# Kernel optimization log

Measured on AMD Instinct MI355X. Metric: run time of the kernel, lower is better.

Reference implementation:

```python
import jax, jax.numpy as jnp
import numpy as np

HQ, HKV, HD = 32, 8, 64
G = HQ // HKV
SCALE = HD ** -0.5


def _rope(x, offset=0):
    # x: [B, L, H, hd], interleaved-pair rotary as in the torch module
    B, L, H, hd = x.shape
    inv = 1.0 / (10000.0 ** (jnp.arange(0, hd, 2, dtype=jnp.float32) / hd))  # [hd/2]
    pos = jnp.arange(offset, offset + L, dtype=jnp.float32)
    f = pos[:, None] * inv[None, :]                     # [L, hd/2]
    c = jnp.cos(f)[None, :, None, :]
    s = jnp.sin(f)[None, :, None, :]
    x1, x2 = x[..., 0::2], x[..., 1::2]
    out = jnp.stack([x1 * c - x2 * s, x1 * s + x2 * c], axis=-1)  # [B,L,H,hd/2,2]
    return out.reshape(x.shape)


def setup_inputs() -> dict:
    key = jax.random.key(0)
    ks = jax.random.split(key, 5)
    B, L, D = 2, 2048, 2048
    w = 0.02
    return {
        "x": jax.random.normal(ks[0], (B, L, D), dtype=jnp.float32),
        "Wq": jax.random.normal(ks[1], (HQ * HD, D), dtype=jnp.float32) * w,
        "Wk": jax.random.normal(ks[2], (HKV * HD, D), dtype=jnp.float32) * w,
        "Wv": jax.random.normal(ks[3], (HKV * HD, D), dtype=jnp.float32) * w,
        "Wo": jax.random.normal(ks[4], (D, HQ * HD), dtype=jnp.float32) * w,
    }


def reference(x, Wq, Wk, Wv, Wo):
    B, L, D = x.shape
    q = (x @ Wq.T).reshape(B, L, HQ, HD)
    k = (x @ Wk.T).reshape(B, L, HKV, HD)
    v = (x @ Wv.T).reshape(B, L, HKV, HD)
    q = _rope(q)
    k = _rope(k)
    # GQA via broadcasting instead of repeat_interleave:
    # q head i attends kv head i // G -> group axis g
    qh = q.transpose(0, 2, 1, 3).reshape(B, HKV, G, L, HD)  # [B,Hkv,G,L,hd]
    kh = k.transpose(0, 2, 1, 3)                             # [B,Hkv,L,hd]
    vh = v.transpose(0, 2, 1, 3)
    attn = jnp.einsum("bkgqd,bkld->bkgql", qh, kh) * SCALE
    causal = jnp.arange(L)[:, None] >= jnp.arange(L)[None, :]  # kv_len == L
    attn = jnp.where(causal[None, None, None], attn, -jnp.inf)
    p = jax.nn.softmax(attn, axis=-1)
    out = jnp.einsum("bkgql,bkld->bkgqd", p, vh)             # [B,Hkv,G,L,hd]
    out = out.reshape(B, HQ, L, HD).transpose(0, 2, 1, 3).reshape(B, L, HQ * HD)
    return out @ Wo.T
```

## Files before the change

kernel.cpp:

```cpp
#include <hip/hip_runtime.h>
#include <hip/hip_bf16.h>
#include <hip/hip_fp16.h>

typedef unsigned short u16;
typedef __attribute__((ext_vector_type(8))) short     bf16x8;
typedef __attribute__((ext_vector_type(4))) float     f32x4;
typedef __attribute__((ext_vector_type(4))) _Float16  f16x4;
typedef __attribute__((ext_vector_type(8))) _Float16  f16x8;
typedef __attribute__((ext_vector_type(4))) u16       u16x4;

static constexpr int B_ = 2, L_ = 2048, D_ = 2048;
static constexpr int HQ_ = 32, HD_ = 64;
static constexpr int M_ = B_ * L_;
static constexpr int KVD_ = 512;
static constexpr int NQKV_ = D_ + 2 * KVD_;
static constexpr float QSCALE_ = 0.125f * 1.44269504f;

__device__ __forceinline__ u16 f2bf(float x) {
  union { float f; unsigned u; } c; c.f = x;
  unsigned r = c.u + 0x7FFFu + ((c.u >> 16) & 1u);
  return (u16)(r >> 16);
}
__device__ __forceinline__ float bf2f(u16 x) {
  union { unsigned u; float f; } c; c.u = ((unsigned)x) << 16;
  return c.f;
}

__global__ void cvt5_kernel(const float* __restrict__ s0, const float* __restrict__ s1,
                            const float* __restrict__ s2, const float* __restrict__ s3,
                            const float* __restrict__ s4, u16* __restrict__ dst,
                            long p0, long p1, long p2, long p3, long ntot4) {
  long i = (long)blockIdx.x * blockDim.x + threadIdx.x;
  if (i >= ntot4) return;
  const float* src; long lo;
  if (i < p0)      { src = s0; lo = i; }
  else if (i < p1) { src = s1; lo = i - p0; }
  else if (i < p2) { src = s2; lo = i - p1; }
  else if (i < p3) { src = s3; lo = i - p2; }
  else             { src = s4; lo = i - p3; }
  float4 v = ((const float4*)src)[lo];
  u16x4 w;
  w[0] = f2bf(v.x); w[1] = f2bf(v.y); w[2] = f2bf(v.z); w[3] = f2bf(v.w);
  ((u16x4*)dst)[i] = w;
}

__device__ __forceinline__ void gld_lds16(const void* g, void* l) {
  __builtin_amdgcn_global_load_lds((const __attribute__((address_space(1))) void*)g,
                                   (__attribute__((address_space(3))) void*)l, 16, 0, 0);
}

template <int OUTM>
__global__ __launch_bounds__(256) void gemm_bt(const u16* __restrict__ A,
                                               const u16* __restrict__ Bm,
                                               void* __restrict__ C,
                                               int M, int N, int K) {
  __shared__ u16 As[128 * 32];
  __shared__ u16 Bs[128 * 32];
  const int tid  = threadIdx.x;
  const int lane = tid & 63;
  const int wave = tid >> 6;
  const int wr = wave >> 1, wc = wave & 1;
  const long bm = (long)blockIdx.y * 128;
  const long bn = (long)blockIdx.x * 128;

  f32x4 acc[4][4] = {};

  const u16* ag = A + (bm + wave * 32 + (lane >> 2)) * (long)K + (lane & 3) * 8;
  const u16* bg = Bm + (bn + wave * 32 + (lane >> 2)) * (long)K + (lane & 3) * 8;
  u16* asl0 = &As[wave * 1024];
  u16* asl1 = &As[wave * 1024 + 512];
  u16* bsl0 = &Bs[wave * 1024];
  u16* bsl1 = &Bs[wave * 1024 + 512];

  for (int k0 = 0; k0 < K; k0 += 32) {
    __syncthreads();
    gld_lds16(ag + k0, asl0);
    gld_lds16(ag + k0 + 16 * (long)K, asl1);
    gld_lds16(bg + k0, bsl0);
    gld_lds16(bg + k0 + 16 * (long)K, bsl1);
    __syncthreads();
    bf16x8 af[4], bf[4];
    const int kx = (lane >> 4) * 8;
#pragma unroll
    for (int m = 0; m < 4; ++m)
      af[m] = *(const bf16x8*)&As[(wr * 64 + m * 16 + (lane & 15)) * 32 + kx];
#pragma unroll
    for (int n = 0; n < 4; ++n)
      bf[n] = *(const bf16x8*)&Bs[(wc * 64 + n * 16 + (lane & 15)) * 32 + kx];
#pragma unroll
    for (int m = 0; m < 4; ++m)
#pragma unroll
      for (int n = 0; n < 4; ++n)
        acc[m][n] = __builtin_amdgcn_mfma_f32_16x16x32_bf16(af[m], bf[n], acc[m][n], 0, 0, 0);
  }

  const int cw = lane & 15;
  const int rg = (lane >> 4) * 4;
#pragma unroll
  for (int m = 0; m < 4; ++m) {
    const long row0 = bm + wr * 64 + m * 16 + rg;
#pragma unroll
    for (int n = 0; n < 4; ++n) {
      const long col = bn + wc * 64 + n * 16 + cw;
      if (OUTM == 2) {
#pragma unroll
        for (int j = 0; j < 4; ++j)
          ((float*)C)[(row0 + j) * (long)N + col] = acc[m][n][j];
      } else {
        u16* qb = (u16*)C;
        u16* kb = qb + (long)M_ * D_;
        _Float16* vt = (_Float16*)(kb + (long)M_ * KVD_);
        if (bn < D_) {
#pragma unroll
          for (int j = 0; j < 4; ++j)
            qb[(row0 + j) * (long)D_ + col] = f2bf(acc[m][n][j]);
        } else if (bn < D_ + KVD_) {
#pragma unroll
          for (int j = 0; j < 4; ++j)
            kb[(row0 + j) * (long)KVD_ + (col - D_)] = f2bf(acc[m][n][j]);
        } else {
          f16x4 w;
#pragma unroll
          for (int j = 0; j < 4; ++j) w[j] = (_Float16)acc[m][n][j];
          const long off3 = (row0 >> 11) * ((long)KVD_ * L_) + (col - D_ - KVD_) * (long)L_ + (row0 & (L_ - 1));
          *(f16x4*)(vt + off3) = w;
        }
      }
    }
  }
}

__global__ void rope_kernel(u16* __restrict__ buf, int npairs_row, float outscale, int total) {
  int idx = blockIdx.x * blockDim.x + threadIdx.x;
  if (idx >= total) return;
  int row = idx / npairs_row;
  int cp  = idx - row * npairs_row;
  int i   = cp & 31;
  int pos = row & (L_ - 1);
  float f = (float)pos * __expf(-(float)(2 * i) * (9.210340372f / 64.f));
  float s, c;
  __sincosf(f, &s, &c);
  long off = (long)row * (npairs_row * 2) + (cp >> 5) * 64 + (i << 1);
  float x1 = bf2f(buf[off]), x2 = bf2f(buf[off + 1]);
  buf[off]     = f2bf((x1 * c - x2 * s) * outscale);
  buf[off + 1] = f2bf((x1 * s + x2 * c) * outscale);
}

__device__ __forceinline__ void sm_step(f32x4 (&s)[4], f16x4 (&pb)[4], float& l_run,
                                        int kv0, int qbase, int qq, int kg) {
  if (kv0 + 63 > qbase) {
    const int qrow = qbase + qq;
    const int kb0 = kv0 + 4 * kg;
#pragma unroll
    for (int ks = 0; ks < 4; ++ks)
#pragma unroll
      for (int j = 0; j < 4; ++j)
        s[ks][j] = (kb0 + ks * 16 + j <= qrow) ? s[ks][j] : -INFINITY;
  }
  float ps[4];
#pragma unroll
  for (int ks = 0; ks < 4; ++ks) {
    const float p0 = exp2f(s[ks][0]), p1 = exp2f(s[ks][1]);
    const float p2 = exp2f(s[ks][2]), p3 = exp2f(s[ks][3]);
    pb[ks][0] = (_Float16)p0; pb[ks][1] = (_Float16)p1;
    pb[ks][2] = (_Float16)p2; pb[ks][3] = (_Float16)p3;
    ps[ks] = (p0 + p1) + (p2 + p3);
  }
  l_run += (ps[0] + ps[1]) + (ps[2] + ps[3]);
}

__device__ __forceinline__ void pv_step(const f16x4 (&va)[4][4], const f16x4 (&pb)[4],
                                        f32x4 (&acc)[4]) {
  __builtin_amdgcn_s_setprio(1);
#pragma unroll
  for (int ks = 0; ks < 4; ++ks)
#pragma unroll
    for (int dt = 0; dt < 4; ++dt)
      acc[dt] = __builtin_amdgcn_mfma_f32_16x16x16f16(va[ks][dt], pb[ks], acc[dt], 0, 0, 0);
  __builtin_amdgcn_s_setprio(0);
}

__global__ __launch_bounds__(256) void attn_kernel(const u16* __restrict__ Q,
                                                   const u16* __restrict__ Kb,
                                                   const _Float16* __restrict__ VT,
                                                   u16* __restrict__ O) {
  const int bid = blockIdx.x;
  const int kvh = bid & 7;
  const int idx = bid >> 3;
  const int q4  = idx & 15;
  const int hh  = (idx >> 4) & 3;
  const int b   = idx >> 6;
  const int s4  = idx >> 5;
  int qblk;
  if (s4 == 0)      qblk = q4;
  else if (s4 == 1) qblk = 15 - q4;
  else if (s4 == 2) qblk = (q4 + 8) & 15;
  else              qblk = (7 - q4) & 15;
  const int h = kvh * 4 + hh;

  const int tid = threadIdx.x, lane = tid & 63, wave = tid >> 6;
  const int qq = lane & 15, kg = lane >> 4;

  __shared__ u16      Ks[2][2][64 * 64];
  __shared__ _Float16 Vs[2][2][64 * 64];

  const int q0 = qblk * 128 + wave * 32;
  bf16x8 qf[2][2];
#pragma unroll
  for (int f = 0; f < 2; ++f) {
    const u16* qp = Q + (long)(b * L_ + q0 + f * 16 + qq) * D_ + h * 64 + kg * 8;
    qf[f][0] = *(const bf16x8*)qp;
    qf[f][1] = *(const bf16x8*)(qp + 32);
  }
  f32x4 acc0[4] = {}, acc1[4] = {};
  float l0 = 0.f, l1 = 0.f;
  const int ntiles = qblk + 1;

  const u16*      kbase = Kb + (long)b * L_ * KVD_ + kvh * 64;
  const _Float16* vbase = VT + (long)b * ((long)KVD_ * L_) + (long)(kvh * 64) * L_;

  auto stage = [&](int buf, int t) {
    const long kv0 = (long)t * 128;
#pragma unroll
    for (int v = 0; v < 2; ++v) {
#pragma unroll
      for (int i = 0; i < 2; ++i) {
        const int c   = tid + i * 256;
        const int row = c >> 3;
        const int s16 = (c & 7) ^ (row & 7);
        gld_lds16(kbase + (kv0 + v * 64 + row) * KVD_ + s16 * 8, (u16*)&Ks[buf][v][0] + c * 8);
        gld_lds16(vbase + (long)row * L_ + kv0 + v * 64 + s16 * 8, (_Float16*)&Vs[buf][v][0] + c * 8);
      }
    }
  };

  stage(0, 0);
  __syncthreads();

  for (int t = 0; t < ntiles; ++t) {
    const int buf = t & 1;
    if (t + 1 < ntiles) stage(buf ^ 1, t + 1);

    const int sw = (qq & 7) << 4;
#pragma unroll
    for (int v = 0; v < 2; ++v) {
      const int kv0 = t * 128 + v * 64;
      const char* ksb = (const char*)&Ks[buf][v][0];
      const char* vsb = (const char*)&Vs[buf][v][0];

      bf16x8 kf[4][2];
#pragma unroll
      for (int ks = 0; ks < 4; ++ks) {
        const int rowb = (ks * 16 + qq) * 128;
        kf[ks][0] = *(const bf16x8*)(ksb + rowb + ((kg * 16) ^ sw));
        kf[ks][1] = *(const bf16x8*)(ksb + rowb + ((kg * 16 + 64) ^ sw));
      }
      f16x4 va[4][4];
#pragma unroll
      for (int ks = 0; ks < 4; ++ks)
#pragma unroll
        for (int dt = 0; dt < 4; ++dt)
          va[ks][dt] = *(const f16x4*)(vsb + (dt * 16 + qq) * 128 + ((ks * 32 + kg * 8) ^ sw));

      f32x4 s[4];
      f16x4 pb[4];
#pragma unroll
      for (int ks = 0; ks < 4; ++ks) {
        f32x4 z = {};
        z = __builtin_amdgcn_mfma_f32_16x16x32_bf16(kf[ks][0], qf[0][0], z, 0, 0, 0);
        z = __builtin_amdgcn_mfma_f32_16x16x32_bf16(kf[ks][1], qf[0][1], z, 0, 0, 0);
        s[ks] = z;
      }
      sm_step(s, pb, l0, kv0, q0, qq, kg);
      pv_step(va, pb, acc0);
#pragma unroll
      for (int ks = 0; ks < 4; ++ks) {
        f32x4 z = {};
        z = __builtin_amdgcn_mfma_f32_16x16x32_bf16(kf[ks][0], qf[1][0], z, 0, 0, 0);
        z = __builtin_amdgcn_mfma_f32_16x16x32_bf16(kf[ks][1], qf[1][1], z, 0, 0, 0);
        s[ks] = z;
      }
      sm_step(s, pb, l1, kv0, q0 + 16, qq, kg);
      pv_step(va, pb, acc1);
    }

    __syncthreads();
  }

#pragma unroll
  for (int f = 0; f < 2; ++f) {
    const f32x4* accw = f ? acc1 : acc0;
    float lr = f ? l1 : l0;
    lr += __shfl_xor(lr, 16);
    lr += __shfl_xor(lr, 32);
    const float inv_l = 1.f / lr;
    const long row = (long)(b * L_ + q0 + f * 16 + qq);
#pragma unroll
    for (int dt = 0; dt < 4; ++dt) {
      u16x4 w2;
#pragma unroll
      for (int j = 0; j < 4; ++j) w2[j] = f2bf(accw[dt][j] * inv_l);
      *(u16x4*)(O + row * D_ + h * 64 + dt * 16 + 4 * kg) = w2;
    }
  }
}

extern "C" void kernel_launch(void* const* d_in, const int* in_sizes, int n_in,
                              void* d_out, int out_size, void* d_ws, size_t ws_size,
                              hipStream_t stream) {
  const float* x  = (const float*)d_in[0];
  const float* Wq = (const float*)d_in[1];
  const float* Wk = (const float*)d_in[2];
  const float* Wv = (const float*)d_in[3];
  const float* Wo = (const float*)d_in[4];
  float* out = (float*)d_out;
  char* ws = (char*)d_ws;
  size_t off = 0;
  auto alloc = [&](size_t bytes) -> void* {
    void* p = ws + off; off += (bytes + 255) & ~(size_t)255; return p;
  };
  u16* x_bf  = (u16*)alloc((size_t)M_ * D_ * 2);
  u16* wq_bf = (u16*)alloc((size_t)D_ * D_ * 2);
  u16* wk_bf = (u16*)alloc((size_t)KVD_ * D_ * 2);
  u16* wv_bf = (u16*)alloc((size_t)KVD_ * D_ * 2);
  u16* wo_bf = (u16*)alloc((size_t)D_ * D_ * 2);
  u16* qb = (u16*)alloc((size_t)M_ * D_ * 2);
  u16* kb = (u16*)alloc((size_t)M_ * KVD_ * 2);
  _Float16* vt = (_Float16*)alloc((size_t)M_ * KVD_ * 2);
  u16* ao = (u16*)alloc((size_t)M_ * D_ * 2);

  {
    const long q0 = (long)M_ * D_ / 4;
    const long q1 = q0 + (long)D_ * D_ / 4;
    const long q2 = q1 + (long)KVD_ * D_ / 4;
    const long q3 = q2 + (long)KVD_ * D_ / 4;
    const long qt = q3 + (long)D_ * D_ / 4;
    cvt5_kernel<<<(int)((qt + 255) / 256), 256, 0, stream>>>(x, Wq, Wk, Wv, Wo, x_bf,
                                                             q0, q1, q2, q3, qt);
  }

  dim3 blk(256);
  gemm_bt<4><<<dim3(NQKV_ / 128, M_ / 128), blk, 0, stream>>>(x_bf, wq_bf, qb, M_, NQKV_, D_);

  {
    int totq = M_ * (D_ / 2);
    rope_kernel<<<(totq + 255) / 256, blk, 0, stream>>>(qb, D_ / 2, QSCALE_, totq);
    int totk = M_ * (KVD_ / 2);
    rope_kernel<<<(totk + 255) / 256, blk, 0, stream>>>(kb, KVD_ / 2, 1.0f, totk);
  }

  attn_kernel<<<dim3(1024), dim3(256), 0, stream>>>(qb, kb, vt, ao);

  gemm_bt<2><<<dim3(D_ / 128, M_ / 128), blk, 0, stream>>>(ao, wo_bf, (void*)out, M_, D_, D_);
}
```

Before: 256.3 us.

## Fuse RoPE into QKV GEMM epilogue and double attention query block size

Applies the rotary embedding and query scaling inside the QKV GEMM epilogue, pairing adjacent columns with a lane shuffle, and removes the two standalone rope kernels. This avoids an extra read-modify-write pass over Q and K and two launches. The attention kernel now uses 512-thread blocks covering 256 query rows, so each K/V tile staged into shared memory serves twice as many queries. Waves whose causal range ends early skip compute but still join the barriers. Load balance changes to a simple per-batch reversed ordering over 512 blocks, which may hurt tail balance.

```diff
diff --git a/kernel.cpp b/kernel.cpp
--- a/kernel.cpp
+++ b/kernel.cpp
@@ -20,10 +20,6 @@
   union { float f; unsigned u; } c; c.f = x;
   unsigned r = c.u + 0x7FFFu + ((c.u >> 16) & 1u);
   return (u16)(r >> 16);
-}
-__device__ __forceinline__ float bf2f(u16 x) {
-  union { unsigned u; float f; } c; c.u = ((unsigned)x) << 16;
-  return c.f;
 }
 
 __global__ void cvt5_kernel(const float* __restrict__ s0, const float* __restrict__ s1,
@@ -110,14 +106,21 @@
         u16* qb = (u16*)C;
         u16* kb = qb + (long)M_ * D_;
         _Float16* vt = (_Float16*)(kb + (long)M_ * KVD_);
-        if (bn < D_) {
-#pragma unroll
-          for (int j = 0; j < 4; ++j)
-            qb[(row0 + j) * (long)D_ + col] = f2bf(acc[m][n][j]);
-        } else if (bn < D_ + KVD_) {
-#pragma unroll
-          for (int j = 0; j < 4; ++j)
-            kb[(row0 + j) * (long)KVD_ + (col - D_)] = f2bf(acc[m][n][j]);
+        if (bn < D_ + KVD_) {
+          const int i2 = (int)(col & 63) >> 1;
+          const float inv = __expf(-(float)(2 * i2) * (9.210340372f / 64.f));
+          const bool odd = (cw & 1);
+#pragma unroll
+          for (int j = 0; j < 4; ++j) {
+            const float v = acc[m][n][j];
+            const float p = __shfl_xor(v, 1);
+            const int pos = (int)((row0 + j) & (L_ - 1));
+            float sn, cs;
+            __sincosf((float)pos * inv, &sn, &cs);
+            const float r = odd ? (p * sn + v * cs) : (v * cs - p * sn);
+            if (bn < D_) qb[(row0 + j) * (long)D_ + col] = f2bf(r * QSCALE_);
+            else         kb[(row0 + j) * (long)KVD_ + (col - D_)] = f2bf(r);
+          }
         } else {
           f16x4 w;
 #pragma unroll
@@ -130,22 +133,6 @@
   }
 }
 
-__global__ void rope_kernel(u16* __restrict__ buf, int npairs_row, float outscale, int total) {
-  int idx = blockIdx.x * blockDim.x + threadIdx.x;
-  if (idx >= total) return;
-  int row = idx / npairs_row;
-  int cp  = idx - row * npairs_row;
-  int i   = cp & 31;
-  int pos = row & (L_ - 1);
-  float f = (float)pos * __expf(-(float)(2 * i) * (9.210340372f / 64.f));
-  float s, c;
-  __sincosf(f, &s, &c);
-  long off = (long)row * (npairs_row * 2) + (cp >> 5) * 64 + (i << 1);
-  float x1 = bf2f(buf[off]), x2 = bf2f(buf[off + 1]);
-  buf[off]     = f2bf((x1 * c - x2 * s) * outscale);
-  buf[off + 1] = f2bf((x1 * s + x2 * c) * outscale);
-}
-
 __device__ __forceinline__ void sm_step(f32x4 (&s)[4], f16x4 (&pb)[4], float& l_run,
                                         int kv0, int qbase, int qq, int kg) {
   if (kv0 + 63 > qbase) {
@@ -180,22 +167,17 @@
   __builtin_amdgcn_s_setprio(0);
 }
 
-__global__ __launch_bounds__(256) void attn_kernel(const u16* __restrict__ Q,
+__global__ __launch_bounds__(512) void attn_kernel(const u16* __restrict__ Q,
                                                    const u16* __restrict__ Kb,
                                                    const _Float16* __restrict__ VT,
                                                    u16* __restrict__ O) {
   const int bid = blockIdx.x;
   const int kvh = bid & 7;
   const int idx = bid >> 3;
-  const int q4  = idx & 15;
-  const int hh  = (idx >> 4) & 3;
-  const int b   = idx >> 6;
-  const int s4  = idx >> 5;
-  int qblk;
-  if (s4 == 0)      qblk = q4;
-  else if (s4 == 1) qblk = 15 - q4;
-  else if (s4 == 2) qblk = (q4 + 8) & 15;
-  else              qblk = (7 - q4) & 15;
+  const int q3  = idx & 7;
+  const int hh  = (idx >> 3) & 3;
+  const int b   = idx >> 5;
+  const int qblk = b ? (7 - q3) : q3;
   const int h = kvh * 4 + hh;
 
   const int tid = threadIdx.x, lane = tid & 63, wave = tid >> 6;
@@ -204,7 +186,7 @@
   __shared__ u16      Ks[2][2][64 * 64];
   __shared__ _Float16 Vs[2][2][64 * 64];
 
-  const int q0 = qblk * 128 + wave * 32;
+  const int q0 = qblk * 256 + wave * 32;
   bf16x8 qf[2][2];
 #pragma unroll
   for (int f = 0; f < 2; ++f) {
@@ -214,7 +196,8 @@
   }
   f32x4 acc0[4] = {}, acc1[4] = {};
   float l0 = 0.f, l1 = 0.f;
-  const int ntiles = qblk + 1;
+  const int ntiles  = 2 * qblk + 2;
+  const int myTiles = ((q0 + 31) >> 7) + 1;
 
   const u16*      kbase = Kb + (long)b * L_ * KVD_ + kvh * 64;
   const _Float16* vbase = VT + (long)b * ((long)KVD_ * L_) + (long)(kvh * 64) * L_;
@@ -223,14 +206,11 @@
     const long kv0 = (long)t * 128;
 #pragma unroll
     for (int v = 0; v < 2; ++v) {
-#pragma unroll
-      for (int i = 0; i < 2; ++i) {
-        const int c   = tid + i * 256;
-        const int row = c >> 3;
-        const int s16 = (c & 7) ^ (row & 7);
-        gld_lds16(kbase + (kv0 + v * 64 + row) * KVD_ + s16 * 8, (u16*)&Ks[buf][v][0] + c * 8);
-        gld_lds16(vbase + (long)row * L_ + kv0 + v * 64 + s16 * 8, (_Float16*)&Vs[buf][v][0] + c * 8);
-      }
+      const int c   = tid;
+      const int row = c >> 3;
+      const int s16 = (c & 7) ^ (row & 7);
+      gld_lds16(kbase + (kv0 + v * 64 + row) * KVD_ + s16 * 8, (u16*)&Ks[buf][v][0] + c * 8);
+      gld_lds16(vbase + (long)row * L_ + kv0 + v * 64 + s16 * 8, (_Float16*)&Vs[buf][v][0] + c * 8);
     }
   };
 
@@ -241,47 +221,49 @@
     const int buf = t & 1;
     if (t + 1 < ntiles) stage(buf ^ 1, t + 1);
 
-    const int sw = (qq & 7) << 4;
-#pragma unroll
-    for (int v = 0; v < 2; ++v) {
-      const int kv0 = t * 128 + v * 64;
-      const char* ksb = (const char*)&Ks[buf][v][0];
-      const char* vsb = (const char*)&Vs[buf][v][0];
-
-      bf16x8 kf[4][2];
-#pragma unroll
-      for (int ks = 0; ks < 4; ++ks) {
-        const int rowb = (ks * 16 + qq) * 128;
-        kf[ks][0] = *(const bf16x8*)(ksb + rowb + ((kg * 16) ^ sw));
-        kf[ks][1] = *(const bf16x8*)(ksb + rowb + ((kg * 16 + 64) ^ sw));
+    if (t < myTiles) {
+      const int sw = (qq & 7) << 4;
+#pragma unroll
+      for (int v = 0; v < 2; ++v) {
+        const int kv0 = t * 128 + v * 64;
+        const char* ksb = (const char*)&Ks[buf][v][0];
+        const char* vsb = (const char*)&Vs[buf][v][0];
+
+        bf16x8 kf[4][2];
+#pragma unroll
+        for (int ks = 0; ks < 4; ++ks) {
+          const int rowb = (ks * 16 + qq) * 128;
+          kf[ks][0] = *(const bf16x8*)(ksb + rowb + ((kg * 16) ^ sw));
+          kf[ks][1] = *(const bf16x8*)(ksb + rowb + ((kg * 16 + 64) ^ sw));
+        }
+        f16x4 va[4][4];
+#pragma unroll
+        for (int ks = 0; ks < 4; ++ks)
+#pragma unroll
+          for (int dt = 0; dt < 4; ++dt)
+            va[ks][dt] = *(const f16x4*)(vsb + (dt * 16 + qq) * 128 + ((ks * 32 + kg * 8) ^ sw));
+
+        f32x4 s[4];
+        f16x4 pb[4];
+#pragma unroll
+        for (int ks = 0; ks < 4; ++ks) {
+          f32x4 z = {};
+          z = __builtin_amdgcn_mfma_f32_16x16x32_bf16(kf[ks][0], qf[0][0], z, 0, 0, 0);
+          z = __builtin_amdgcn_mfma_f32_16x16x32_bf16(kf[ks][1], qf[0][1], z, 0, 0, 0);
+          s[ks] = z;
+        }
+        sm_step(s, pb, l0, kv0, q0, qq, kg);
+        pv_step(va, pb, acc0);
+#pragma unroll
+        for (int ks = 0; ks < 4; ++ks) {
+          f32x4 z = {};
+          z = __builtin_amdgcn_mfma_f32_16x16x32_bf16(kf[ks][0], qf[1][0], z, 0, 0, 0);
+          z = __builtin_amdgcn_mfma_f32_16x16x32_bf16(kf[ks][1], qf[1][1], z, 0, 0, 0);
+          s[ks] = z;
+        }
+        sm_step(s, pb, l1, kv0, q0 + 16, qq, kg);
+        pv_step(va, pb, acc1);
       }
-      f16x4 va[4][4];
-#pragma unroll
-      for (int ks = 0; ks < 4; ++ks)
-#pragma unroll
-        for (int dt = 0; dt < 4; ++dt)
-          va[ks][dt] = *(const f16x4*)(vsb + (dt * 16 + qq) * 128 + ((ks * 32 + kg * 8) ^ sw));
-
-      f32x4 s[4];
-      f16x4 pb[4];
-#pragma unroll
-      for (int ks = 0; ks < 4; ++ks) {
-        f32x4 z = {};
-        z = __builtin_amdgcn_mfma_f32_16x16x32_bf16(kf[ks][0], qf[0][0], z, 0, 0, 0);
-        z = __builtin_amdgcn_mfma_f32_16x16x32_bf16(kf[ks][1], qf[0][1], z, 0, 0, 0);
-        s[ks] = z;
-      }
-      sm_step(s, pb, l0, kv0, q0, qq, kg);
-      pv_step(va, pb, acc0);
-#pragma unroll
-      for (int ks = 0; ks < 4; ++ks) {
-        f32x4 z = {};
-        z = __builtin_amdgcn_mfma_f32_16x16x32_bf16(kf[ks][0], qf[1][0], z, 0, 0, 0);
-        z = __builtin_amdgcn_mfma_f32_16x16x32_bf16(kf[ks][1], qf[1][1], z, 0, 0, 0);
-        s[ks] = z;
-      }
-      sm_step(s, pb, l1, kv0, q0 + 16, qq, kg);
-      pv_step(va, pb, acc1);
     }
 
     __syncthreads();
@@ -342,14 +324,7 @@
   dim3 blk(256);
   gemm_bt<4><<<dim3(NQKV_ / 128, M_ / 128), blk, 0, stream>>>(x_bf, wq_bf, qb, M_, NQKV_, D_);
 
-  {
-    int totq = M_ * (D_ / 2);
-    rope_kernel<<<(totq + 255) / 256, blk, 0, stream>>>(qb, D_ / 2, QSCALE_, totq);
-    int totk = M_ * (KVD_ / 2);
-    rope_kernel<<<(totk + 255) / 256, blk, 0, stream>>>(kb, KVD_ / 2, 1.0f, totk);
-  }
-
-  attn_kernel<<<dim3(1024), dim3(256), 0, stream>>>(qb, kb, vt, ao);
+  attn_kernel<<<dim3(512), dim3(512), 0, stream>>>(qb, kb, vt, ao);
 
   gemm_bt<2><<<dim3(D_ / 128, M_ / 128), blk, 0, stream>>>(ao, wo_bf, (void*)out, M_, D_, D_);
 }
```

Result: no change. 257.9 us (+0.6%).
